# Optimization experiments

Hardware: AMD Instinct MI355X
Metric: run time of the kernel (lower is better)

Reference implementation:

```python
import jax, jax.numpy as jnp
import numpy as np

B, C_IN, IMG = 4, 1, 256
E, P = 800, 4            # embed_size, patch_size
H, DH, M = 8, 64, 64     # heads, dim_head=heads**2, num_landmarks
N = (IMG // P) ** 2      # 4096 tokens
OUT = 256                # output_size
RESK = 33                # lucidrains residual depthwise conv kernel
BN_EPS = 1e-5
LN_EPS = 1e-5
PINV_ITERS = 6


def setup_inputs() -> dict:
    key = jax.random.key(0)
    ks = iter(jax.random.split(key, 32))
    def nrm(shape, s=0.02):
        return jax.random.normal(next(ks), shape, jnp.float32) * s
    inp = {"x": jax.random.normal(next(ks), (B, C_IN, IMG, IMG), jnp.float32)}
    # conv stack: (in, out, kernel); last conv has stride=P, padding=0
    for i, (ci, co, kk) in enumerate([(C_IN, 64, 3), (64, 128, 3), (128, 256, 3), (256, E, P)]):
        inp[f"w{i}"] = nrm((co, ci, kk, kk), 0.05)
        inp[f"b{i}"] = jnp.zeros((co,), jnp.float32)
        inp[f"g{i}"] = jnp.ones((co,), jnp.float32)    # BN gamma
        inp[f"be{i}"] = jnp.zeros((co,), jnp.float32)  # BN beta
        inp[f"mu{i}"] = nrm((co,), 0.1)                # BN running mean
        inp[f"var{i}"] = jax.random.uniform(next(ks), (co,), jnp.float32, 0.5, 1.5)
    inp["qkv_w"] = nrm((E, 3 * H * DH))      # to_qkv (no bias)
    inp["out_w"] = nrm((H * DH, E))          # to_out linear
    inp["out_b"] = jnp.zeros((E,), jnp.float32)
    inp["res_w"] = nrm((H, 1, RESK, 1), 0.05)  # depthwise residual conv over token dim
    inp["ln_g"] = jnp.ones((E,), jnp.float32)
    inp["ln_b"] = jnp.zeros((E,), jnp.float32)
    inp["head_w"] = nrm((E, OUT * OUT // N))   # Linear(800, 16)
    inp["head_b"] = jnp.zeros((OUT * OUT // N,), jnp.float32)
    return inp


def conv2d(x, w, b, stride, pad):
    y = jax.lax.conv_general_dilated(x, w, (stride, stride), [(pad, pad), (pad, pad)],
                                     dimension_numbers=("NCHW", "OIHW", "NCHW"))
    return y + b[None, :, None, None]


def bn(x, g, be, mu, var):
    s = g * jax.lax.rsqrt(var + BN_EPS)  # eval-mode BatchNorm
    return x * s[None, :, None, None] + (be - mu * s)[None, :, None, None]


def moore_penrose_pinv(a, iters=PINV_ITERS):
    I = jnp.eye(a.shape[-1], dtype=a.dtype)
    z = jnp.swapaxes(a, -1, -2) / (jnp.max(jnp.abs(a).sum(-1)) * jnp.max(jnp.abs(a).sum(-2)))
    for _ in range(iters):
        az = a @ z
        z = 0.25 * z @ (13.0 * I - az @ (15.0 * I - az @ (7.0 * I - az)))
    return z


def reference(x, w0, b0, g0, be0, mu0, var0, w1, b1, g1, be1, mu1, var1,
              w2, b2, g2, be2, mu2, var2, w3, b3, g3, be3, mu3, var3,
              qkv_w, out_w, out_b, res_w, ln_g, ln_b, head_w, head_b):
    # ---- PatchEmbedConv ----
    h = x
    blocks = [(w0, b0, g0, be0, mu0, var0, 1, 1), (w1, b1, g1, be1, mu1, var1, 1, 1),
              (w2, b2, g2, be2, mu2, var2, 1, 1), (w3, b3, g3, be3, mu3, var3, P, 0)]
    for w, b, g, be, mu, var, st, pd in blocks:
        h = jax.nn.relu(bn(conv2d(h, w, b, st, pd), g, be, mu, var))
    tok = h.reshape(B, E, N).transpose(0, 2, 1)  # [B, N, E]

    # ---- NystromAttention (n % m == 0, so no front padding needed) ----
    qkv = tok @ qkv_w  # [B, N, 3*H*DH]
    q, k, v = [t.reshape(B, N, H, DH).transpose(0, 2, 1, 3) for t in jnp.split(qkv, 3, axis=-1)]
    q = q * (DH ** -0.5)
    l = N // M
    q_l = q.reshape(B, H, M, l, DH).mean(3)  # landmark means over consecutive blocks
    k_l = k.reshape(B, H, M, l, DH).mean(3)
    a1 = jax.nn.softmax(jnp.einsum("bhnd,bhmd->bhnm", q, k_l), axis=-1)    # [B,H,N,M]
    a2 = jax.nn.softmax(jnp.einsum("bhmd,bhkd->bhmk", q_l, k_l), axis=-1)  # [B,H,M,M]
    a3 = jax.nn.softmax(jnp.einsum("bhmd,bhnd->bhmn", q_l, k), axis=-1)    # [B,H,M,N]
    out = (a1 @ moore_penrose_pinv(a2)) @ (a3 @ v)  # [B,H,N,DH]
    # residual depthwise conv over the token dim of v (groups = heads)
    res = jax.lax.conv_general_dilated(v, res_w, (1, 1), [(RESK // 2, RESK // 2), (0, 0)],
                                       dimension_numbers=("NCHW", "OIHW", "NCHW"),
                                       feature_group_count=H)
    out = out + res
    out = out.transpose(0, 2, 1, 3).reshape(B, N, H * DH)
    out = out @ out_w + out_b  # [B, N, E]

    # ---- LayerNorm ----
    mu_t = out.mean(-1, keepdims=True)
    var_t = out.var(-1, keepdims=True)
    out = (out - mu_t) * jax.lax.rsqrt(var_t + LN_EPS) * ln_g + ln_b

    # ---- reconstruction head ----
    y = jax.nn.sigmoid(out @ head_w + head_b)  # [B, N, OUT*OUT/N]
    return y.reshape(-1, 1, OUT, OUT)
```

## Files before the change

### kernel.cpp

```cpp
#include <hip/hip_runtime.h>

#define DI __device__ __forceinline__

constexpr float BN_EPS_C = 1e-5f;
constexpr float LN_EPS_C = 1e-5f;

typedef _Float16 half8 __attribute__((ext_vector_type(8)));
typedef float f32x4 __attribute__((ext_vector_type(4)));

constexpr size_t B_H0   = 0;
constexpr size_t B_H1   = 8388608;
constexpr size_t B_H2   = 25165824;
constexpr size_t B_Q    = 25165824;
constexpr size_t B_K    = 41943040;
constexpr size_t B_V    = 58720256;
constexpr size_t B_KT   = 75497472;
constexpr size_t B_ATT  = 92274688;
constexpr size_t B_LNB  = 25165824;
constexpr size_t B_TOK  = 159383552;
constexpr size_t B_WP1  = 185597952;
constexpr size_t B_WP2  = 185745408;
constexpr size_t B_WP3  = 186335232;
constexpr size_t B_QKVT = 192888832;
constexpr size_t B_OWT  = 195346432;
constexpr size_t B_QL   = 196165632;
constexpr size_t B_KL   = 196689920;
constexpr size_t B_KLH  = 197214208;
constexpr size_t B_A2   = 197476352;
constexpr size_t B_PV   = 198000640;
constexpr size_t B_W2T  = 198524928;
constexpr size_t B_A3V  = 198787072;
constexpr size_t B_SCAL = 199311360;
constexpr size_t B_HWH  = 199311424;

DI float blockReduceSum(float v) {
  #pragma unroll
  for (int o = 32; o; o >>= 1) v += __shfl_xor(v, o);
  __shared__ float red[4];
  int w = threadIdx.x >> 6;
  __syncthreads();
  if ((threadIdx.x & 63) == 0) red[w] = v;
  __syncthreads();
  return red[0] + red[1] + red[2] + red[3];
}

template <int LP, int RP>
DI void mm16(const float* L, const float* R, int r0, int c0, float reg[4][4]) {
  #pragma unroll
  for (int i = 0; i < 4; ++i)
    #pragma unroll
    for (int j = 0; j < 4; ++j) reg[i][j] = 0.f;
  for (int dd = 0; dd < 64; ++dd) {
    float l[4], r[4];
    #pragma unroll
    for (int i = 0; i < 4; ++i) l[i] = L[(size_t)(r0 + i) * LP + dd];
    #pragma unroll
    for (int j = 0; j < 4; ++j) r[j] = R[(size_t)dd * RP + c0 + j];
    #pragma unroll
    for (int i = 0; i < 4; ++i)
      #pragma unroll
      for (int j = 0; j < 4; ++j) reg[i][j] = fmaf(l[i], r[j], reg[i][j]);
  }
}

__global__ void k_init(float* scal) {
  if (threadIdx.x < 2) scal[threadIdx.x] = 0.f;
}

__global__ void k_pack_w(const float* __restrict__ src, _Float16* __restrict__ dst,
                         int CO, int CI, int Q) {
  int i = blockIdx.x * 256 + threadIdx.x;
  if (i >= CO * CI * Q) return;
  int q = i % Q, ci = (i / Q) % CI, co = i / (Q * CI);
  dst[((size_t)co * Q + q) * CI + ci] = (_Float16)src[i];
}

__global__ void k_pack_t(const float* __restrict__ src, _Float16* __restrict__ dst,
                         int K, int N) {
  int i = blockIdx.x * 256 + threadIdx.x;
  if (i >= K * N) return;
  int n = i % N, k = i / N;
  dst[(size_t)n * K + k] = (_Float16)src[i];
}

__global__ __launch_bounds__(256) void k_conv0(
    const float* __restrict__ xb, const float* __restrict__ w0, const float* __restrict__ b0,
    const float* __restrict__ g0, const float* __restrict__ be0, const float* __restrict__ mu0,
    const float* __restrict__ var0, _Float16* __restrict__ h0) {
  const int t = threadIdx.x, co = t & 63, xg = t >> 6;
  const int y = blockIdx.x;
  float wreg[9];
  #pragma unroll
  for (int q = 0; q < 9; ++q) wreg[q] = w0[co * 9 + q];
  float s = g0[co] * rsqrtf(var0[co] + BN_EPS_C);
  float sh = fmaf(b0[co] - mu0[co], s, be0[co]);
  for (int xl = 0; xl < 64; ++xl) {
    int xx = xg * 64 + xl;
    float acc = 0.f;
    #pragma unroll
    for (int dy = 0; dy < 3; ++dy) {
      int yy = y + dy - 1;
      if ((unsigned)yy >= 256u) continue;
      #pragma unroll
      for (int dx = 0; dx < 3; ++dx) {
        int xi = xx + dx - 1;
        if ((unsigned)xi >= 256u) continue;
        acc = fmaf(wreg[dy * 3 + dx], xb[yy * 256 + xi], acc);
      }
    }
    float v = fmaxf(fmaf(acc, s, sh), 0.f);
    h0[((size_t)y * 256 + xx) * 64 + co] = (_Float16)v;
  }
}

template <int CI>
__global__ __launch_bounds__(256) void k_convs(
    const _Float16* __restrict__ in, const _Float16* __restrict__ wp,
    const float* __restrict__ bias, const float* __restrict__ g, const float* __restrict__ be,
    const float* __restrict__ mu, const float* __restrict__ var,
    _Float16* __restrict__ out, int CO, int NCT) {
  __shared__ _Float16 Ab[2][128 * 40];
  __shared__ _Float16 Bb[2][128 * 40];
  constexpr int CPQ = CI / 32;
  constexpr int NCK = 9 * CPQ;
  const int t = threadIdx.x;
  const int bid = blockIdx.x;
  const int xcd = bid & 7, slot = bid >> 3;
  const int pj = slot / NCT, cc = slot % NCT;
  const int p = pj * 8 + xcd;
  const int r0 = p * 128, c0 = cc * 128;

  const int ma = t >> 2, kga = t & 3;
  int ry[2], rx[2];
  #pragma unroll
  for (int s = 0; s < 2; ++s) {
    int r = r0 + ma + s * 64;
    ry[s] = r >> 8;
    rx[s] = r & 255;
  }
  const _Float16* baseB[2];
  #pragma unroll
  for (int s = 0; s < 2; ++s)
    baseB[s] = wp + (size_t)(c0 + ma + s * 64) * 9 * CI + kga * 8;
  const int wo = ma * 40 + kga * 8;

  auto loadA = [&](int s, int ck) -> half8 {
    int q = ck / CPQ, coff = (ck % CPQ) * 32;
    int yy = ry[s] + q / 3 - 1;
    int xx = rx[s] + q % 3 - 1;
    half8 a = {};
    if ((unsigned)yy < 256u && (unsigned)xx < 256u)
      a = *reinterpret_cast<const half8*>(in + ((size_t)yy * 256 + xx) * CI + coff + kga * 8);
    return a;
  };

  {
    half8 a0 = loadA(0, 0), a1 = loadA(1, 0);
    half8 b0v = *reinterpret_cast<const half8*>(baseB[0]);
    half8 b1v = *reinterpret_cast<const half8*>(baseB[1]);
    *reinterpret_cast<half8*>(&Ab[0][wo]) = a0;
    *reinterpret_cast<half8*>(&Ab[0][wo + 2560]) = a1;
    *reinterpret_cast<half8*>(&Bb[0][wo]) = b0v;
    *reinterpret_cast<half8*>(&Bb[0][wo + 2560]) = b1v;
  }
  __syncthreads();

  const int w = t >> 6, lo = t & 15, hi = (t >> 4) & 3;
  const int wm = w >> 1, wn = w & 1;
  const int roA = (wm * 64 + lo) * 40 + 8 * hi;
  const int roB = (wn * 64 + lo) * 40 + 8 * hi;
  f32x4 acc[4][4] = {};

  for (int ck = 0; ck < NCK; ++ck) {
    const int cur = ck & 1;
    const bool more = (ck + 1 < NCK);
    half8 rA0, rA1, rB0, rB1;
    if (more) {
      rA0 = loadA(0, ck + 1);
      rA1 = loadA(1, ck + 1);
      rB0 = *reinterpret_cast<const half8*>(baseB[0] + (ck + 1) * 32);
      rB1 = *reinterpret_cast<const half8*>(baseB[1] + (ck + 1) * 32);
    }
    half8 af[4], bf[4];
    #pragma unroll
    for (int mi = 0; mi < 4; ++mi)
      af[mi] = *reinterpret_cast<const half8*>(&Ab[cur][roA + mi * 640]);
    #pragma unroll
    for (int ni = 0; ni < 4; ++ni)
      bf[ni] = *reinterpret_cast<const half8*>(&Bb[cur][roB + ni * 640]);
    #pragma unroll
    for (int mi = 0; mi < 4; ++mi)
      #pragma unroll
      for (int ni = 0; ni < 4; ++ni)
        acc[mi][ni] = __builtin_amdgcn_mfma_f32_16x16x32_f16(af[mi], bf[ni], acc[mi][ni], 0, 0, 0);
    if (more) {
      *reinterpret_cast<half8*>(&Ab[cur ^ 1][wo]) = rA0;
      *reinterpret_cast<half8*>(&Ab[cur ^ 1][wo + 2560]) = rA1;
      *reinterpret_cast<half8*>(&Bb[cur ^ 1][wo]) = rB0;
      *reinterpret_cast<half8*>(&Bb[cur ^ 1][wo + 2560]) = rB1;
    }
    __syncthreads();
  }

  #pragma unroll
  for (int ni = 0; ni < 4; ++ni) {
    int co = c0 + wn * 64 + ni * 16 + lo;
    float s = g[co] * rsqrtf(var[co] + BN_EPS_C);
    float sh = fmaf(bias[co] - mu[co], s, be[co]);
    #pragma unroll
    for (int mi = 0; mi < 4; ++mi)
      #pragma unroll
      for (int rr = 0; rr < 4; ++rr) {
        int row = r0 + wm * 64 + mi * 16 + hi * 4 + rr;
        float v = fmaxf(fmaf(acc[mi][ni][rr], s, sh), 0.f);
        out[(size_t)row * CO + co] = (_Float16)v;
      }
  }
}

__global__ __launch_bounds__(256) void k_c3(
    const _Float16* __restrict__ h2, const _Float16* __restrict__ wp3,
    const float* __restrict__ b3, const float* __restrict__ g3, const float* __restrict__ be3,
    const float* __restrict__ mu3, const float* __restrict__ var3,
    _Float16* __restrict__ tok) {
  __shared__ _Float16 Abuf[2][128 * 40];
  __shared__ _Float16 Bbuf[2][160 * 40];
  const int t = threadIdx.x;
  const int bid = blockIdx.x;
  const int xcd = bid & 7, slot = bid >> 3;
  const int pj = slot / 5, cc = slot % 5;
  const int p = pj * 8 + xcd;
  const int r0 = p * 128, c0 = cc * 160;
  const int img = r0 >> 12;
  const _Float16* h2i = h2 + (size_t)img * 16777216;

  const int ma = t >> 2, kga = t & 3;
  const _Float16* baseA[2];
  #pragma unroll
  for (int s = 0; s < 2; ++s) {
    int m = ma + s * 64;
    int r = r0 + m;
    int py = (r & 4095) >> 6, px = r & 63;
    baseA[s] = h2i + ((size_t)py * 1024 + px * 4) * 256 + kga * 8;
  }
  const _Float16* baseB[3];
  #pragma unroll
  for (int s = 0; s < 3; ++s) {
    int cb = ma + s * 64;
    baseB[s] = wp3 + (size_t)(c0 + (cb < 160 ? cb : 159)) * 4096 + kga * 8;
  }
  const int wo = ma * 40 + kga * 8;

  const int w = t >> 6, lo = t & 15, hi = (t >> 4) & 3;
  const int wm = w >> 1, wn = w & 1;
  const int roA = (wm * 64 + lo) * 40 + 8 * hi;
  const int roB = (wn * 80 + lo) * 40 + 8 * hi;

  f32x4 acc[4][5] = {};

  {
    half8 a0 = *reinterpret_cast<const half8*>(baseA[0]);
    half8 a1 = *reinterpret_cast<const half8*>(baseA[1]);
    half8 b0v = *reinterpret_cast<const half8*>(baseB[0]);
    half8 b1v = *reinterpret_cast<const half8*>(baseB[1]);
    *reinterpret_cast<half8*>(&Abuf[0][wo]) = a0;
    *reinterpret_cast<half8*>(&Abuf[0][wo + 2560]) = a1;
    *reinterpret_cast<half8*>(&Bbuf[0][wo]) = b0v;
    *reinterpret_cast<half8*>(&Bbuf[0][wo + 2560]) = b1v;
    if (t < 128) {
      half8 b2v = *reinterpret_cast<const half8*>(baseB[2]);
      *reinterpret_cast<half8*>(&Bbuf[0][wo + 5120]) = b2v;
    }
  }
  __syncthreads();

  for (int ck = 0; ck < 128; ++ck) {
    const int cur = ck & 1;
    const bool more = (ck + 1 < 128);
    half8 rA0, rA1, rB0, rB1, rB2;
    if (more) {
      const int kn = (ck + 1) << 5;
      const int q = kn >> 8, qk = kn & 255;
      const int aoff = (q >> 2) * 65536 + (q & 3) * 256 + qk;
      rA0 = *reinterpret_cast<const half8*>(baseA[0] + aoff);
      rA1 = *reinterpret_cast<const half8*>(baseA[1] + aoff);
      rB0 = *reinterpret_cast<const half8*>(baseB[0] + kn);
      rB1 = *reinterpret_cast<const half8*>(baseB[1] + kn);
      if (t < 128) rB2 = *reinterpret_cast<const half8*>(baseB[2] + kn);
    }
    half8 af[4], bf[5];
    #pragma unroll
    for (int mi = 0; mi < 4; ++mi)
      af[mi] = *reinterpret_cast<const half8*>(&Abuf[cur][roA + mi * 640]);
    #pragma unroll
    for (int ni = 0; ni < 5; ++ni)
      bf[ni] = *reinterpret_cast<const half8*>(&Bbuf[cur][roB + ni * 640]);
    #pragma unroll
    for (int mi = 0; mi < 4; ++mi)
      #pragma unroll
      for (int ni = 0; ni < 5; ++ni)
        acc[mi][ni] = __builtin_amdgcn_mfma_f32_16x16x32_f16(af[mi], bf[ni], acc[mi][ni], 0, 0, 0);
    if (more) {
      *reinterpret_cast<half8*>(&Abuf[cur ^ 1][wo]) = rA0;
      *reinterpret_cast<half8*>(&Abuf[cur ^ 1][wo + 2560]) = rA1;
      *reinterpret_cast<half8*>(&Bbuf[cur ^ 1][wo]) = rB0;
      *reinterpret_cast<half8*>(&Bbuf[cur ^ 1][wo + 2560]) = rB1;
      if (t < 128) *reinterpret_cast<half8*>(&Bbuf[cur ^ 1][wo + 5120]) = rB2;
    }
    __syncthreads();
  }

  #pragma unroll
  for (int ni = 0; ni < 5; ++ni) {
    int col = c0 + wn * 80 + ni * 16 + lo;
    float s = g3[col] * rsqrtf(var3[col] + BN_EPS_C);
    float sh = fmaf(b3[col] - mu3[col], s, be3[col]);
    #pragma unroll
    for (int mi = 0; mi < 4; ++mi)
      #pragma unroll
      for (int rr = 0; rr < 4; ++rr) {
        int row = r0 + wm * 64 + mi * 16 + hi * 4 + rr;
        float v = fmaxf(fmaf(acc[mi][ni][rr], s, sh), 0.f);
        tok[(size_t)row * 800 + col] = (_Float16)v;
      }
  }
}

__global__ __launch_bounds__(256) void k_qkv_s(
    const _Float16* __restrict__ tok, const _Float16* __restrict__ qkvT,
    _Float16* __restrict__ qx, _Float16* __restrict__ kx, _Float16* __restrict__ vx) {
  __shared__ _Float16 Ab[2][128 * 40];
  __shared__ _Float16 Bb[2][128 * 40];
  const int t = threadIdx.x;
  const int bid = blockIdx.x;
  const int xcd = bid & 7, slot = bid >> 3;
  const int pj = slot / 12, cc = slot % 12;
  const int p = pj * 8 + xcd;
  const int r0 = p * 128, c0 = cc * 128;

  const int ma = t >> 2, kga = t & 3;
  const _Float16* baseA[2];
  const _Float16* baseB[2];
  #pragma unroll
  for (int s = 0; s < 2; ++s) {
    baseA[s] = tok + (size_t)(r0 + ma + s * 64) * 800 + kga * 8;
    baseB[s] = qkvT + (size_t)(c0 + ma + s * 64) * 800 + kga * 8;
  }
  const int wo = ma * 40 + kga * 8;

  {
    half8 a0 = *reinterpret_cast<const half8*>(baseA[0]);
    half8 a1 = *reinterpret_cast<const half8*>(baseA[1]);
    half8 b0v = *reinterpret_cast<const half8*>(baseB[0]);
    half8 b1v = *reinterpret_cast<const half8*>(baseB[1]);
    *reinterpret_cast<half8*>(&Ab[0][wo]) = a0;
    *reinterpret_cast<half8*>(&Ab[0][wo + 2560]) = a1;
    *reinterpret_cast<half8*>(&Bb[0][wo]) = b0v;
    *reinterpret_cast<half8*>(&Bb[0][wo + 2560]) = b1v;
  }
  __syncthreads();

  const int w = t >> 6, lo = t & 15, hi = (t >> 4) & 3;
  const int wm = w >> 1, wn = w & 1;
  const int roA = (wm * 64 + lo) * 40 + 8 * hi;
  const int roB = (wn * 64 + lo) * 40 + 8 * hi;
  f32x4 acc[4][4] = {};

  for (int ck = 0; ck < 25; ++ck) {
    const int cur = ck & 1;
    const bool more = (ck + 1 < 25);
    half8 rA0, rA1, rB0, rB1;
    if (more) {
      const int kn = (ck + 1) * 32;
      rA0 = *reinterpret_cast<const half8*>(baseA[0] + kn);
      rA1 = *reinterpret_cast<const half8*>(baseA[1] + kn);
      rB0 = *reinterpret_cast<const half8*>(baseB[0] + kn);
      rB1 = *reinterpret_cast<const half8*>(baseB[1] + kn);
    }
    half8 af[4], bf[4];
    #pragma unroll
    for (int mi = 0; mi < 4; ++mi)
      af[mi] = *reinterpret_cast<const half8*>(&Ab[cur][roA + mi * 640]);
    #pragma unroll
    for (int ni = 0; ni < 4; ++ni)
      bf[ni] = *reinterpret_cast<const half8*>(&Bb[cur][roB + ni * 640]);
    #pragma unroll
    for (int mi = 0; mi < 4; ++mi)
      #pragma unroll
      for (int ni = 0; ni < 4; ++ni)
        acc[mi][ni] = __builtin_amdgcn_mfma_f32_16x16x32_f16(af[mi], bf[ni], acc[mi][ni], 0, 0, 0);
    if (more) {
      *reinterpret_cast<half8*>(&Ab[cur ^ 1][wo]) = rA0;
      *reinterpret_cast<half8*>(&Ab[cur ^ 1][wo + 2560]) = rA1;
      *reinterpret_cast<half8*>(&Bb[cur ^ 1][wo]) = rB0;
      *reinterpret_cast<half8*>(&Bb[cur ^ 1][wo + 2560]) = rB1;
    }
    __syncthreads();
  }

  const int seg = cc >> 2;
  const float scale = (seg == 0) ? 0.125f : 1.0f;
  _Float16* dst = (seg == 0) ? qx : (seg == 1) ? kx : vx;
  #pragma unroll
  for (int ni = 0; ni < 4; ++ni) {
    int cseg = (cc & 3) * 128 + wn * 64 + ni * 16 + lo;
    int h = cseg >> 6, d = cseg & 63;
    #pragma unroll
    for (int mi = 0; mi < 4; ++mi)
      #pragma unroll
      for (int rr = 0; rr < 4; ++rr) {
        int row = r0 + wm * 64 + mi * 16 + hi * 4 + rr;
        int b = row >> 12, nn = row & 4095;
        dst[((size_t)(b * 8 + h) * 4096 + nn) * 64 + d] = (_Float16)(acc[mi][ni][rr] * scale);
      }
  }
}

__global__ __launch_bounds__(256) void k_op_s(
    const _Float16* __restrict__ attb, const _Float16* __restrict__ owT,
    const float* __restrict__ ob, _Float16* __restrict__ lnb) {
  __shared__ _Float16 Abuf[2][128 * 40];
  __shared__ _Float16 Bbuf[2][160 * 40];
  const int t = threadIdx.x;
  const int bid = blockIdx.x;
  const int xcd = bid & 7, slot = bid >> 3;
  const int pj = slot / 5, cc = slot % 5;
  const int p = pj * 8 + xcd;
  const int r0 = p * 128, c0 = cc * 160;

  const int ma = t >> 2, kga = t & 3;
  const _Float16* baseA[2];
  #pragma unroll
  for (int s = 0; s < 2; ++s)
    baseA[s] = attb + (size_t)(r0 + ma + s * 64) * 512 + kga * 8;
  const _Float16* baseB[3];
  #pragma unroll
  for (int s = 0; s < 3; ++s) {
    int cb = ma + s * 64;
    baseB[s] = owT + (size_t)(c0 + (cb < 160 ? cb : 159)) * 512 + kga * 8;
  }
  const int wo = ma * 40 + kga * 8;

  const int w = t >> 6, lo = t & 15, hi = (t >> 4) & 3;
  const int wm = w >> 1, wn = w & 1;
  const int roA = (wm * 64 + lo) * 40 + 8 * hi;
  const int roB = (wn * 80 + lo) * 40 + 8 * hi;

  f32x4 acc[4][5] = {};

  {
    half8 a0 = *reinterpret_cast<const half8*>(baseA[0]);
    half8 a1 = *reinterpret_cast<const half8*>(baseA[1]);
    half8 b0v = *reinterpret_cast<const half8*>(baseB[0]);
    half8 b1v = *reinterpret_cast<const half8*>(baseB[1]);
    *reinterpret_cast<half8*>(&Abuf[0][wo]) = a0;
    *reinterpret_cast<half8*>(&Abuf[0][wo + 2560]) = a1;
    *reinterpret_cast<half8*>(&Bbuf[0][wo]) = b0v;
    *reinterpret_cast<half8*>(&Bbuf[0][wo + 2560]) = b1v;
    if (t < 128) {
      half8 b2v = *reinterpret_cast<const half8*>(baseB[2]);
      *reinterpret_cast<half8*>(&Bbuf[0][wo + 5120]) = b2v;
    }
  }
  __syncthreads();

  for (int ck = 0; ck < 16; ++ck) {
    const int cur = ck & 1;
    const bool more = (ck + 1 < 16);
    half8 rA0, rA1, rB0, rB1, rB2;
    if (more) {
      const int kn = (ck + 1) << 5;
      rA0 = *reinterpret_cast<const half8*>(baseA[0] + kn);
      rA1 = *reinterpret_cast<const half8*>(baseA[1] + kn);
      rB0 = *reinterpret_cast<const half8*>(baseB[0] + kn);
      rB1 = *reinterpret_cast<const half8*>(baseB[1] + kn);
      if (t < 128) rB2 = *reinterpret_cast<const half8*>(baseB[2] + kn);
    }
    half8 af[4], bf[5];
    #pragma unroll
    for (int mi = 0; mi < 4; ++mi)
      af[mi] = *reinterpret_cast<const half8*>(&Abuf[cur][roA + mi * 640]);
    #pragma unroll
    for (int ni = 0; ni < 5; ++ni)
      bf[ni] = *reinterpret_cast<const half8*>(&Bbuf[cur][roB + ni * 640]);
    #pragma unroll
    for (int mi = 0; mi < 4; ++mi)
      #pragma unroll
      for (int ni = 0; ni < 5; ++ni)
        acc[mi][ni] = __builtin_amdgcn_mfma_f32_16x16x32_f16(af[mi], bf[ni], acc[mi][ni], 0, 0, 0);
    if (more) {
      *reinterpret_cast<half8*>(&Abuf[cur ^ 1][wo]) = rA0;
      *reinterpret_cast<half8*>(&Abuf[cur ^ 1][wo + 2560]) = rA1;
      *reinterpret_cast<half8*>(&Bbuf[cur ^ 1][wo]) = rB0;
      *reinterpret_cast<half8*>(&Bbuf[cur ^ 1][wo + 2560]) = rB1;
      if (t < 128) *reinterpret_cast<half8*>(&Bbuf[cur ^ 1][wo + 5120]) = rB2;
    }
    __syncthreads();
  }

  #pragma unroll
  for (int ni = 0; ni < 5; ++ni) {
    int col = c0 + wn * 80 + ni * 16 + lo;
    float bv = ob[col];
    #pragma unroll
    for (int mi = 0; mi < 4; ++mi)
      #pragma unroll
      for (int rr = 0; rr < 4; ++rr) {
        int row = r0 + wm * 64 + mi * 16 + hi * 4 + rr;
        lnb[(size_t)row * 800 + col] = (_Float16)(acc[mi][ni][rr] + bv);
      }
  }
}

__global__ __launch_bounds__(256) void k_transpose(const _Float16* __restrict__ kx,
                                                   _Float16* __restrict__ kT) {
  __shared__ _Float16 tile[64 * 66];
  const int bh = blockIdx.y, n0 = blockIdx.x * 64;
  const _Float16* src = kx + ((size_t)bh * 4096 + n0) * 64;
  const int t = threadIdx.x;
  #pragma unroll
  for (int u = 0; u < 16; ++u) {
    int e = t + u * 256;
    int r = e >> 6, d = e & 63;
    tile[d * 66 + r] = src[e];
  }
  __syncthreads();
  _Float16* dst = kT + (size_t)bh * 262144 + n0;
  #pragma unroll
  for (int u = 0; u < 16; ++u) {
    int e = t + u * 256;
    int d = e >> 6, j = e & 63;
    dst[(size_t)d * 4096 + j] = tile[d * 66 + j];
  }
}

__global__ __launch_bounds__(64) void k_landmark(
    const _Float16* __restrict__ qx, const _Float16* __restrict__ kx,
    float* __restrict__ ql, float* __restrict__ kl, _Float16* __restrict__ klh) {
  const int d = threadIdx.x;
  const int m = blockIdx.x, bh = blockIdx.y;
  const _Float16* qp = qx + ((size_t)bh * 4096 + m * 64) * 64 + d;
  const _Float16* kp = kx + ((size_t)bh * 4096 + m * 64) * 64 + d;
  float sq = 0.f, sk = 0.f;
  #pragma unroll 8
  for (int j = 0; j < 64; ++j) {
    sq += (float)qp[(size_t)j * 64];
    sk += (float)kp[(size_t)j * 64];
  }
  sq *= (1.f / 64.f);
  sk *= (1.f / 64.f);
  ql[((size_t)bh * 64 + m) * 64 + d] = sq;
  kl[((size_t)bh * 64 + m) * 64 + d] = sk;
  klh[((size_t)bh * 64 + m) * 64 + d] = (_Float16)sk;
}

__global__ __launch_bounds__(64) void k_a2(
    const float* __restrict__ ql, const float* __restrict__ kl,
    float* __restrict__ a2, float* __restrict__ scal) {
  __shared__ float sp[64 * 65];
  const int bh = blockIdx.x, t = threadIdx.x;
  const float* qr = ql + ((size_t)bh * 64 + t) * 64;
  const float* kb = kl + (size_t)bh * 4096;
  float mx = -1e30f;
  for (int c = 0; c < 64; ++c) {
    float acc = 0.f;
    #pragma unroll 8
    for (int dd = 0; dd < 64; ++dd) acc = fmaf(qr[dd], kb[c * 64 + dd], acc);
    sp[t * 65 + c] = acc;
    mx = fmaxf(mx, acc);
  }
  float sum = 0.f;
  for (int c = 0; c < 64; ++c) {
    float e = expf(sp[t * 65 + c] - mx);
    sp[t * 65 + c] = e;
    sum += e;
  }
  float inv = 1.f / sum;
  float rs = 0.f;
  for (int c = 0; c < 64; ++c) {
    float p = sp[t * 65 + c] * inv;
    sp[t * 65 + c] = p;
    a2[(size_t)bh * 4096 + t * 64 + c] = p;
    rs += p;
  }
  atomicMax(reinterpret_cast<int*>(scal), __float_as_int(rs));
  __syncthreads();
  float cs = 0.f;
  for (int r = 0; r < 64; ++r) cs += sp[r * 65 + t];
  atomicMax(reinterpret_cast<int*>(scal) + 1, __float_as_int(cs));
}

__global__ __launch_bounds__(256) void k_a3v(
    const float* __restrict__ ql, const _Float16* __restrict__ kT,
    const _Float16* __restrict__ vx, float* __restrict__ a3v) {
  __shared__ float sq[64];
  __shared__ float sP[4096];
  __shared__ float red[4];
  __shared__ float red2[4][64];
  const int t = threadIdx.x;
  const int m = blockIdx.x, bh = blockIdx.y;
  if (t < 64) sq[t] = ql[((size_t)bh * 64 + m) * 64 + t];
  __syncthreads();
  const _Float16* kb = kT + (size_t)bh * 262144;
  float sc[16];
  #pragma unroll
  for (int i = 0; i < 16; ++i) sc[i] = 0.f;
  for (int dd = 0; dd < 64; ++dd) {
    float qv = sq[dd];
    const _Float16* kr = kb + (size_t)dd * 4096 + t;
    #pragma unroll
    for (int i = 0; i < 16; ++i) sc[i] = fmaf(qv, (float)kr[i * 256], sc[i]);
  }
  float mx = sc[0];
  #pragma unroll
  for (int i = 1; i < 16; ++i) mx = fmaxf(mx, sc[i]);
  #pragma unroll
  for (int o = 32; o; o >>= 1) mx = fmaxf(mx, __shfl_xor(mx, o));
  if ((t & 63) == 0) red[t >> 6] = mx;
  __syncthreads();
  mx = fmaxf(fmaxf(red[0], red[1]), fmaxf(red[2], red[3]));
  __syncthreads();
  float sum = 0.f;
  #pragma unroll
  for (int i = 0; i < 16; ++i) {
    sc[i] = expf(sc[i] - mx);
    sum += sc[i];
  }
  #pragma unroll
  for (int o = 32; o; o >>= 1) sum += __shfl_xor(sum, o);
  if ((t & 63) == 0) red[t >> 6] = sum;
  __syncthreads();
  sum = red[0] + red[1] + red[2] + red[3];
  float inv = 1.f / sum;
  #pragma unroll
  for (int i = 0; i < 16; ++i) sP[t + i * 256] = sc[i] * inv;
  __syncthreads();
  const int d = t & 63, seg = t >> 6;
  const _Float16* vb = vx + (size_t)bh * 262144;
  float acc = 0.f;
  for (int n = seg * 1024; n < seg * 1024 + 1024; ++n)
    acc = fmaf(sP[n], (float)vb[(size_t)n * 64 + d], acc);
  red2[seg][d] = acc;
  __syncthreads();
  if (seg == 0)
    a3v[((size_t)bh * 64 + m) * 64 + d] = red2[0][d] + red2[1][d] + red2[2][d] + red2[3][d];
}

__global__ __launch_bounds__(256) void k_pinv(
    const float* __restrict__ a2g, const float* __restrict__ scal, float* __restrict__ pv) {
  __shared__ float z[64 * 65];
  __shared__ float az[64 * 65];
  __shared__ float tb[64 * 65];
  const int bh = blockIdx.x, t = threadIdx.x;
  const int r0 = (t >> 4) << 2, c0 = (t & 15) << 2;
  const float* ag = a2g + (size_t)bh * 4096;
  const float denom = 1.f / (scal[0] * scal[1]);
  #pragma unroll
  for (int i = 0; i < 4; ++i)
    #pragma unroll
    for (int j = 0; j < 4; ++j)
      z[(r0 + i) * 65 + c0 + j] = ag[(c0 + j) * 64 + r0 + i] * denom;
  __syncthreads();
  float reg[4][4], val[4][4];
  for (int it = 0; it < 6; ++it) {
    mm16<64, 65>(ag, z, r0, c0, reg);
    #pragma unroll
    for (int i = 0; i < 4; ++i)
      #pragma unroll
      for (int j = 0; j < 4; ++j) az[(r0 + i) * 65 + c0 + j] = reg[i][j];
    __syncthreads();
    mm16<65, 65>(az, az, r0, c0, reg);
    #pragma unroll
    for (int i = 0; i < 4; ++i)
      #pragma unroll
      for (int j = 0; j < 4; ++j)
        tb[(r0 + i) * 65 + c0 + j] = 7.f * az[(r0 + i) * 65 + c0 + j] - reg[i][j];
    __syncthreads();
    mm16<65, 65>(az, tb, r0, c0, reg);
    #pragma unroll
    for (int i = 0; i < 4; ++i)
      #pragma unroll
      for (int j = 0; j < 4; ++j)
        val[i][j] = 15.f * az[(r0 + i) * 65 + c0 + j] - reg[i][j];
    __syncthreads();
    #pragma unroll
    for (int i = 0; i < 4; ++i)
      #pragma unroll
      for (int j = 0; j < 4; ++j) tb[(r0 + i) * 65 + c0 + j] = val[i][j];
    __syncthreads();
    mm16<65, 65>(z, tb, r0, c0, reg);
    #pragma unroll
    for (int i = 0; i < 4; ++i)
      #pragma unroll
      for (int j = 0; j < 4; ++j)
        val[i][j] = 0.25f * (13.f * z[(r0 + i) * 65 + c0 + j] - reg[i][j]);
    __syncthreads();
    #pragma unroll
    for (int i = 0; i < 4; ++i)
      #pragma unroll
      for (int j = 0; j < 4; ++j) z[(r0 + i) * 65 + c0 + j] = val[i][j];
    __syncthreads();
  }
  #pragma unroll
  for (int i = 0; i < 4; ++i)
    #pragma unroll
    for (int j = 0; j < 4; ++j)
      pv[(size_t)bh * 4096 + (r0 + i) * 64 + c0 + j] = z[(r0 + i) * 65 + c0 + j];
}

__global__ __launch_bounds__(256) void k_w2(
    const float* __restrict__ pv, const float* __restrict__ a3v, _Float16* __restrict__ w2t) {
  const int bh = blockIdx.x, t = threadIdx.x;
  const int r0 = (t >> 4) << 2, c0 = (t & 15) << 2;
  float reg[4][4];
  mm16<64, 64>(pv + (size_t)bh * 4096, a3v + (size_t)bh * 4096, r0, c0, reg);
  #pragma unroll
  for (int i = 0; i < 4; ++i)
    #pragma unroll
    for (int j = 0; j < 4; ++j)
      w2t[(size_t)bh * 4096 + (c0 + j) * 64 + (r0 + i)] = (_Float16)reg[i][j];
}

__global__ __launch_bounds__(256) void k_combine_m(
    const _Float16* __restrict__ qx, const _Float16* __restrict__ klh,
    const _Float16* __restrict__ w2t, const _Float16* __restrict__ vx,
    const float* __restrict__ rw, _Float16* __restrict__ att) {
  __shared__ _Float16 sP[64 * 72];
  __shared__ _Float16 sVT[64 * 104];
  __shared__ _Float16 sT[64 * 104];
  __shared__ float sR[33];
  const int t = threadIdx.x, w = t >> 6, lo = t & 15, hi = (t >> 4) & 3;
  const int n0 = blockIdx.x * 64;
  const int h = blockIdx.y, b = blockIdx.z, bh = b * 8 + h;
  if (t < 33) sR[t] = rw[h * 33 + t];
  __syncthreads();
  const _Float16* vb = vx + (size_t)bh * 262144;
  #pragma unroll
  for (int u = 0; u < 24; ++u) {
    int e = t + u * 256;
    int r = e >> 6, d = e & 63;
    int nn = n0 - 16 + r;
    sVT[d * 104 + r] = ((unsigned)nn < 4096u) ? vb[(size_t)nn * 64 + d] : (_Float16)0.f;
  }
  #pragma unroll
  for (int u = 0; u < 24; ++u) {
    int e = t + u * 256;
    int r = e % 96, i = e / 96;
    int j = r - i;
    sT[i * 104 + r] = (j >= 0 && j < 33) ? (_Float16)sR[j] : (_Float16)0.f;
  }
  f32x4 sa[4] = {};
  const _Float16* qp = qx + ((size_t)bh * 4096 + n0 + w * 16 + lo) * 64 + 8 * hi;
  const _Float16* klp = klh + (size_t)bh * 4096;
  #pragma unroll
  for (int c = 0; c < 2; ++c) {
    half8 a = *reinterpret_cast<const half8*>(qp + 32 * c);
    #pragma unroll
    for (int ct = 0; ct < 4; ++ct) {
      half8 bf = *reinterpret_cast<const half8*>(klp + (size_t)(ct * 16 + lo) * 64 + 8 * hi + 32 * c);
      sa[ct] = __builtin_amdgcn_mfma_f32_16x16x32_f16(a, bf, sa[ct], 0, 0, 0);
    }
  }
  #pragma unroll
  for (int r = 0; r < 4; ++r) {
    float mx = fmaxf(fmaxf(sa[0][r], sa[1][r]), fmaxf(sa[2][r], sa[3][r]));
    #pragma unroll
    for (int o = 8; o; o >>= 1) mx = fmaxf(mx, __shfl_xor(mx, o));
    float e0 = expf(sa[0][r] - mx), e1 = expf(sa[1][r] - mx);
    float e2 = expf(sa[2][r] - mx), e3 = expf(sa[3][r] - mx);
    float sm = e0 + e1 + e2 + e3;
    #pragma unroll
    for (int o = 8; o; o >>= 1) sm += __shfl_xor(sm, o);
    float inv = 1.f / sm;
    int row = w * 16 + hi * 4 + r;
    sP[row * 72 + lo] = (_Float16)(e0 * inv);
    sP[row * 72 + 16 + lo] = (_Float16)(e1 * inv);
    sP[row * 72 + 32 + lo] = (_Float16)(e2 * inv);
    sP[row * 72 + 48 + lo] = (_Float16)(e3 * inv);
  }
  __syncthreads();
  f32x4 ao[4] = {};
  const _Float16* w2p = w2t + (size_t)bh * 4096;
  #pragma unroll
  for (int c = 0; c < 2; ++c) {
    half8 a = *reinterpret_cast<const half8*>(&sP[(w * 16 + lo) * 72 + 8 * hi + 32 * c]);
    #pragma unroll
    for (int ct = 0; ct < 4; ++ct) {
      half8 bf = *reinterpret_cast<const half8*>(w2p + (size_t)(ct * 16 + lo) * 64 + 8 * hi + 32 * c);
      ao[ct] = __builtin_amdgcn_mfma_f32_16x16x32_f16(a, bf, ao[ct], 0, 0, 0);
    }
  }
  #pragma unroll
  for (int c = 0; c < 3; ++c) {
    half8 a = *reinterpret_cast<const half8*>(&sT[(w * 16 + lo) * 104 + 8 * hi + 32 * c]);
    #pragma unroll
    for (int ct = 0; ct < 4; ++ct) {
      half8 bf = *reinterpret_cast<const half8*>(&sVT[(ct * 16 + lo) * 104 + 8 * hi + 32 * c]);
      ao[ct] = __builtin_amdgcn_mfma_f32_16x16x32_f16(a, bf, ao[ct], 0, 0, 0);
    }
  }
  _Float16* ab = att + ((size_t)b * 4096) * 512 + (size_t)h * 64;
  #pragma unroll
  for (int ct = 0; ct < 4; ++ct)
    #pragma unroll
    for (int r = 0; r < 4; ++r) {
      int n = n0 + w * 16 + hi * 4 + r;
      ab[(size_t)n * 512 + ct * 16 + lo] = (_Float16)ao[ct][r];
    }
}

__global__ __launch_bounds__(256) void k_ln16(
    _Float16* __restrict__ buf, const float* __restrict__ g, const float* __restrict__ bb) {
  const int t = threadIdx.x;
  _Float16* p = buf + (size_t)blockIdx.x * 800;
  float x0 = (float)p[t], x1 = (float)p[t + 256], x2 = (float)p[t + 512];
  float x3 = (t < 32) ? (float)p[t + 768] : 0.f;
  float s = blockReduceSum(x0 + x1 + x2 + x3);
  float mean = s * (1.f / 800.f);
  float d0 = x0 - mean, d1 = x1 - mean, d2 = x2 - mean;
  float d3 = (t < 32) ? x3 - mean : 0.f;
  float s2 = blockReduceSum(d0 * d0 + d1 * d1 + d2 * d2 + d3 * d3);
  float rstd = rsqrtf(s2 * (1.f / 800.f) + LN_EPS_C);
  p[t] = (_Float16)(d0 * rstd * g[t] + bb[t]);
  p[t + 256] = (_Float16)(d1 * rstd * g[t + 256] + bb[t + 256]);
  p[t + 512] = (_Float16)(d2 * rstd * g[t + 512] + bb[t + 512]);
  if (t < 32) p[t + 768] = (_Float16)(d3 * rstd * g[t + 768] + bb[t + 768]);
}

__global__ __launch_bounds__(256) void k_head_m(
    const _Float16* __restrict__ ln, const _Float16* __restrict__ hwh,
    const float* __restrict__ hb, float* __restrict__ out) {
  const int t = threadIdx.x, w = t >> 6, lo = t & 15, hi = (t >> 4) & 3;
  const int row0 = blockIdx.x * 64 + w * 16;
  const _Float16* ap = ln + (size_t)(row0 + lo) * 800 + 8 * hi;
  const _Float16* bp = hwh + (size_t)lo * 800 + 8 * hi;
  f32x4 acc = {};
  #pragma unroll 5
  for (int k = 0; k < 800; k += 32) {
    half8 a = *reinterpret_cast<const half8*>(ap + k);
    half8 b = *reinterpret_cast<const half8*>(bp + k);
    acc = __builtin_amdgcn_mfma_f32_16x16x32_f16(a, b, acc, 0, 0, 0);
  }
  float bv = hb[lo];
  #pragma unroll
  for (int r = 0; r < 4; ++r) {
    int row = row0 + hi * 4 + r;
    out[(size_t)row * 16 + lo] = 1.f / (1.f + expf(-(acc[r] + bv)));
  }
}

extern "C" void kernel_launch(void* const* d_in, const int* in_sizes, int n_in,
                              void* d_out, int out_size, void* d_ws, size_t ws_size,
                              hipStream_t stream) {
  (void)in_sizes; (void)n_in; (void)out_size; (void)ws_size;
  const float* x     = (const float*)d_in[0];
  const float* w0    = (const float*)d_in[1];
  const float* b0    = (const float*)d_in[2];
  const float* g0    = (const float*)d_in[3];
  const float* be0   = (const float*)d_in[4];
  const float* mu0   = (const float*)d_in[5];
  const float* var0  = (const float*)d_in[6];
  const float* w1    = (const float*)d_in[7];
  const float* b1    = (const float*)d_in[8];
  const float* g1    = (const float*)d_in[9];
  const float* be1   = (const float*)d_in[10];
  const float* mu1   = (const float*)d_in[11];
  const float* var1  = (const float*)d_in[12];
  const float* w2c   = (const float*)d_in[13];
  const float* b2    = (const float*)d_in[14];
  const float* g2    = (const float*)d_in[15];
  const float* be2   = (const float*)d_in[16];
  const float* mu2   = (const float*)d_in[17];
  const float* var2  = (const float*)d_in[18];
  const float* w3    = (const float*)d_in[19];
  const float* b3    = (const float*)d_in[20];
  const float* g3    = (const float*)d_in[21];
  const float* be3   = (const float*)d_in[22];
  const float* mu3   = (const float*)d_in[23];
  const float* var3  = (const float*)d_in[24];
  const float* qkvw  = (const float*)d_in[25];
  const float* outw  = (const float*)d_in[26];
  const float* outbv = (const float*)d_in[27];
  const float* resw  = (const float*)d_in[28];
  const float* lng   = (const float*)d_in[29];
  const float* lnbv  = (const float*)d_in[30];
  const float* headw = (const float*)d_in[31];
  const float* headb = (const float*)d_in[32];

  char* wsb = (char*)d_ws;
  _Float16* h0   = (_Float16*)(wsb + B_H0);
  _Float16* h1   = (_Float16*)(wsb + B_H1);
  _Float16* h2   = (_Float16*)(wsb + B_H2);
  _Float16* qb   = (_Float16*)(wsb + B_Q);
  _Float16* kb   = (_Float16*)(wsb + B_K);
  _Float16* vb   = (_Float16*)(wsb + B_V);
  _Float16* kT   = (_Float16*)(wsb + B_KT);
  _Float16* tok  = (_Float16*)(wsb + B_TOK);
  _Float16* attb = (_Float16*)(wsb + B_ATT);
  _Float16* wp1  = (_Float16*)(wsb + B_WP1);
  _Float16* wp2  = (_Float16*)(wsb + B_WP2);
  _Float16* wp3  = (_Float16*)(wsb + B_WP3);
  _Float16* qkvT = (_Float16*)(wsb + B_QKVT);
  _Float16* owT  = (_Float16*)(wsb + B_OWT);
  _Float16* klh  = (_Float16*)(wsb + B_KLH);
  _Float16* w2t  = (_Float16*)(wsb + B_W2T);
  _Float16* hwh  = (_Float16*)(wsb + B_HWH);
  _Float16* lnb16 = (_Float16*)(wsb + B_LNB);
  float* ql   = (float*)(wsb + B_QL);
  float* kl   = (float*)(wsb + B_KL);
  float* a2   = (float*)(wsb + B_A2);
  float* pv   = (float*)(wsb + B_PV);
  float* a3v  = (float*)(wsb + B_A3V);
  float* scal = (float*)(wsb + B_SCAL);

  k_pack_w<<<(128 * 64 * 9 + 255) / 256, 256, 0, stream>>>(w1, wp1, 128, 64, 9);
  k_pack_w<<<(256 * 128 * 9 + 255) / 256, 256, 0, stream>>>(w2c, wp2, 256, 128, 9);
  k_pack_w<<<(800 * 256 * 16 + 255) / 256, 256, 0, stream>>>(w3, wp3, 800, 256, 16);
  k_pack_t<<<(800 * 1536 + 255) / 256, 256, 0, stream>>>(qkvw, qkvT, 800, 1536);
  k_pack_t<<<(512 * 800 + 255) / 256, 256, 0, stream>>>(outw, owT, 512, 800);
  k_pack_t<<<(800 * 16 + 255) / 256, 256, 0, stream>>>(headw, hwh, 800, 16);
  k_init<<<1, 64, 0, stream>>>(scal);

  for (int img = 0; img < 4; ++img) {
    k_conv0<<<dim3(256), 256, 0, stream>>>(
        x + (size_t)img * 65536, w0, b0, g0, be0, mu0, var0, h0);
    k_convs<64><<<dim3(512), 256, 0, stream>>>(
        h0, wp1, b1, g1, be1, mu1, var1, h1, 128, 1);
    k_convs<128><<<dim3(1024), 256, 0, stream>>>(
        h1, wp2, b2, g2, be2, mu2, var2, h2 + (size_t)img * 16777216, 256, 2);
  }
  k_c3<<<dim3(640), 256, 0, stream>>>(h2, wp3, b3, g3, be3, mu3, var3, tok);
  k_qkv_s<<<dim3(1536), 256, 0, stream>>>(tok, qkvT, qb, kb, vb);
  k_transpose<<<dim3(64, 32), 256, 0, stream>>>(kb, kT);
  k_landmark<<<dim3(64, 32), 64, 0, stream>>>(qb, kb, ql, kl, klh);
  k_a2<<<dim3(32), 64, 0, stream>>>(ql, kl, a2, scal);
  k_a3v<<<dim3(64, 32), 256, 0, stream>>>(ql, kT, vb, a3v);
  k_pinv<<<dim3(32), 256, 0, stream>>>(a2, scal, pv);
  k_w2<<<dim3(32), 256, 0, stream>>>(pv, a3v, w2t);
  k_combine_m<<<dim3(64, 8, 4), 256, 0, stream>>>(qb, klh, w2t, vb, resw, attb);
  k_op_s<<<dim3(640), 256, 0, stream>>>(attb, owT, outbv, lnb16);
  k_ln16<<<dim3(16384), 256, 0, stream>>>(lnb16, lng, lnbv);
  k_head_m<<<dim3(256), 256, 0, stream>>>(lnb16, hwh, headb, (float*)d_out);
}
```

Baseline: 1.162 ms.

## Fuse weight packing, write K transposed from QKV GEMM, merge pinv with W2

Merges the six weight-packing kernels and the scalar init into one launch. The QKV GEMM now writes K straight into the transposed [bh,d,n] layout, which removes the separate transpose kernel and the K buffer, and the landmark kernel reads K from that layout with vector loads. The pinv kernel also does the pinv×a3v product from shared memory, which removes the k_w2 launch and the pv round trip. The risk is the QKV epilogue for K, where scattered stores with a 4096 stride may coalesce poorly.

```diff
diff --git a/kernel.cpp b/kernel.cpp
--- a/kernel.cpp
+++ b/kernel.cpp
@@ -12,7 +12,6 @@
 constexpr size_t B_H1   = 8388608;
 constexpr size_t B_H2   = 25165824;
 constexpr size_t B_Q    = 25165824;
-constexpr size_t B_K    = 41943040;
 constexpr size_t B_V    = 58720256;
 constexpr size_t B_KT   = 75497472;
 constexpr size_t B_ATT  = 92274688;
@@ -27,7 +26,6 @@
 constexpr size_t B_KL   = 196689920;
 constexpr size_t B_KLH  = 197214208;
 constexpr size_t B_A2   = 197476352;
-constexpr size_t B_PV   = 198000640;
 constexpr size_t B_W2T  = 198524928;
 constexpr size_t B_A3V  = 198787072;
 constexpr size_t B_SCAL = 199311360;
@@ -63,24 +61,39 @@
   }
 }
 
-__global__ void k_init(float* scal) {
-  if (threadIdx.x < 2) scal[threadIdx.x] = 0.f;
-}
-
-__global__ void k_pack_w(const float* __restrict__ src, _Float16* __restrict__ dst,
-                         int CO, int CI, int Q) {
-  int i = blockIdx.x * 256 + threadIdx.x;
-  if (i >= CO * CI * Q) return;
-  int q = i % Q, ci = (i / Q) % CI, co = i / (Q * CI);
-  dst[((size_t)co * Q + q) * CI + ci] = (_Float16)src[i];
-}
-
-__global__ void k_pack_t(const float* __restrict__ src, _Float16* __restrict__ dst,
-                         int K, int N) {
-  int i = blockIdx.x * 256 + threadIdx.x;
-  if (i >= K * N) return;
-  int n = i % N, k = i / N;
-  dst[(size_t)n * K + k] = (_Float16)src[i];
+__global__ void k_pack_all(
+    const float* __restrict__ w1, const float* __restrict__ w2c, const float* __restrict__ w3,
+    const float* __restrict__ qkvw, const float* __restrict__ outw, const float* __restrict__ headw,
+    _Float16* __restrict__ wp1, _Float16* __restrict__ wp2, _Float16* __restrict__ wp3,
+    _Float16* __restrict__ qkvT, _Float16* __restrict__ owT, _Float16* __restrict__ hwh,
+    float* __restrict__ scal) {
+  size_t i = (size_t)blockIdx.x * 256 + threadIdx.x;
+  if (i < 73728) {
+    int q = i % 9, ci = (i / 9) % 64, co = i / (9 * 64);
+    wp1[((size_t)co * 9 + q) * 64 + ci] = (_Float16)w1[i];
+  } else if (i < 368640) {
+    size_t j = i - 73728;
+    int q = j % 9, ci = (j / 9) % 128, co = j / (9 * 128);
+    wp2[((size_t)co * 9 + q) * 128 + ci] = (_Float16)w2c[j];
+  } else if (i < 3645440) {
+    size_t j = i - 368640;
+    int q = j % 16, ci = (j / 16) % 256, co = j / (16 * 256);
+    wp3[((size_t)co * 16 + q) * 256 + ci] = (_Float16)w3[j];
+  } else if (i < 4874240) {
+    size_t j = i - 3645440;
+    int n = j % 1536, k = j / 1536;
+    qkvT[(size_t)n * 800 + k] = (_Float16)qkvw[j];
+  } else if (i < 5283840) {
+    size_t j = i - 4874240;
+    int n = j % 800, k = j / 800;
+    owT[(size_t)n * 512 + k] = (_Float16)outw[j];
+  } else if (i < 5296640) {
+    size_t j = i - 5283840;
+    int n = j % 16, k = j / 16;
+    hwh[(size_t)n * 800 + k] = (_Float16)headw[j];
+  } else if (i < 5296642) {
+    scal[i - 5296640] = 0.f;
+  }
 }
 
 __global__ __launch_bounds__(256) void k_conv0(
@@ -328,7 +341,7 @@
 
 __global__ __launch_bounds__(256) void k_qkv_s(
     const _Float16* __restrict__ tok, const _Float16* __restrict__ qkvT,
-    _Float16* __restrict__ qx, _Float16* __restrict__ kx, _Float16* __restrict__ vx) {
+    _Float16* __restrict__ qx, _Float16* __restrict__ kTg, _Float16* __restrict__ vx) {
   __shared__ _Float16 Ab[2][128 * 40];
   __shared__ _Float16 Bb[2][128 * 40];
   const int t = threadIdx.x;
@@ -399,20 +412,36 @@
   }
 
   const int seg = cc >> 2;
-  const float scale = (seg == 0) ? 0.125f : 1.0f;
-  _Float16* dst = (seg == 0) ? qx : (seg == 1) ? kx : vx;
-  #pragma unroll
-  for (int ni = 0; ni < 4; ++ni) {
-    int cseg = (cc & 3) * 128 + wn * 64 + ni * 16 + lo;
-    int h = cseg >> 6, d = cseg & 63;
-    #pragma unroll
-    for (int mi = 0; mi < 4; ++mi)
-      #pragma unroll
-      for (int rr = 0; rr < 4; ++rr) {
-        int row = r0 + wm * 64 + mi * 16 + hi * 4 + rr;
-        int b = row >> 12, nn = row & 4095;
-        dst[((size_t)(b * 8 + h) * 4096 + nn) * 64 + d] = (_Float16)(acc[mi][ni][rr] * scale);
-      }
+  if (seg == 1) {
+    #pragma unroll
+    for (int ni = 0; ni < 4; ++ni) {
+      int cseg = (cc & 3) * 128 + wn * 64 + ni * 16 + lo;
+      int h = cseg >> 6, d = cseg & 63;
+      #pragma unroll
+      for (int mi = 0; mi < 4; ++mi)
+        #pragma unroll
+        for (int rr = 0; rr < 4; ++rr) {
+          int row = r0 + wm * 64 + mi * 16 + hi * 4 + rr;
+          int b = row >> 12, nn = row & 4095;
+          kTg[((size_t)(b * 8 + h) * 64 + d) * 4096 + nn] = (_Float16)acc[mi][ni][rr];
+        }
+    }
+  } else {
+    const float scale = (seg == 0) ? 0.125f : 1.0f;
+    _Float16* dst = (seg == 0) ? qx : vx;
+    #pragma unroll
+    for (int ni = 0; ni < 4; ++ni) {
+      int cseg = (cc & 3) * 128 + wn * 64 + ni * 16 + lo;
+      int h = cseg >> 6, d = cseg & 63;
+      #pragma unroll
+      for (int mi = 0; mi < 4; ++mi)
+        #pragma unroll
+        for (int rr = 0; rr < 4; ++rr) {
+          int row = r0 + wm * 64 + mi * 16 + hi * 4 + rr;
+          int b = row >> 12, nn = row & 4095;
+          dst[((size_t)(b * 8 + h) * 4096 + nn) * 64 + d] = (_Float16)(acc[mi][ni][rr] * scale);
+        }
+    }
   }
 }
 
@@ -512,40 +541,21 @@
   }
 }
 
-__global__ __launch_bounds__(256) void k_transpose(const _Float16* __restrict__ kx,
-                                                   _Float16* __restrict__ kT) {
-  __shared__ _Float16 tile[64 * 66];
-  const int bh = blockIdx.y, n0 = blockIdx.x * 64;
-  const _Float16* src = kx + ((size_t)bh * 4096 + n0) * 64;
-  const int t = threadIdx.x;
-  #pragma unroll
-  for (int u = 0; u < 16; ++u) {
-    int e = t + u * 256;
-    int r = e >> 6, d = e & 63;
-    tile[d * 66 + r] = src[e];
-  }
-  __syncthreads();
-  _Float16* dst = kT + (size_t)bh * 262144 + n0;
-  #pragma unroll
-  for (int u = 0; u < 16; ++u) {
-    int e = t + u * 256;
-    int d = e >> 6, j = e & 63;
-    dst[(size_t)d * 4096 + j] = tile[d * 66 + j];
-  }
-}
-
 __global__ __launch_bounds__(64) void k_landmark(
-    const _Float16* __restrict__ qx, const _Float16* __restrict__ kx,
+    const _Float16* __restrict__ qx, const _Float16* __restrict__ kT,
     float* __restrict__ ql, float* __restrict__ kl, _Float16* __restrict__ klh) {
   const int d = threadIdx.x;
   const int m = blockIdx.x, bh = blockIdx.y;
   const _Float16* qp = qx + ((size_t)bh * 4096 + m * 64) * 64 + d;
-  const _Float16* kp = kx + ((size_t)bh * 4096 + m * 64) * 64 + d;
+  const _Float16* kp = kT + ((size_t)bh * 64 + d) * 4096 + m * 64;
   float sq = 0.f, sk = 0.f;
   #pragma unroll 8
-  for (int j = 0; j < 64; ++j) {
-    sq += (float)qp[(size_t)j * 64];
-    sk += (float)kp[(size_t)j * 64];
+  for (int j = 0; j < 64; ++j) sq += (float)qp[(size_t)j * 64];
+  #pragma unroll
+  for (int j = 0; j < 64; j += 8) {
+    half8 kv = *reinterpret_cast<const half8*>(kp + j);
+    #pragma unroll
+    for (int u = 0; u < 8; ++u) sk += (float)kv[u];
   }
   sq *= (1.f / 64.f);
   sk *= (1.f / 64.f);
@@ -647,7 +657,8 @@
 }
 
 __global__ __launch_bounds__(256) void k_pinv(
-    const float* __restrict__ a2g, const float* __restrict__ scal, float* __restrict__ pv) {
+    const float* __restrict__ a2g, const float* __restrict__ scal,
+    const float* __restrict__ a3vg, _Float16* __restrict__ w2t) {
   __shared__ float z[64 * 65];
   __shared__ float az[64 * 65];
   __shared__ float tb[64 * 65];
@@ -701,19 +712,7 @@
       for (int j = 0; j < 4; ++j) z[(r0 + i) * 65 + c0 + j] = val[i][j];
     __syncthreads();
   }
-  #pragma unroll
-  for (int i = 0; i < 4; ++i)
-    #pragma unroll
-    for (int j = 0; j < 4; ++j)
-      pv[(size_t)bh * 4096 + (r0 + i) * 64 + c0 + j] = z[(r0 + i) * 65 + c0 + j];
-}
-
-__global__ __launch_bounds__(256) void k_w2(
-    const float* __restrict__ pv, const float* __restrict__ a3v, _Float16* __restrict__ w2t) {
-  const int bh = blockIdx.x, t = threadIdx.x;
-  const int r0 = (t >> 4) << 2, c0 = (t & 15) << 2;
-  float reg[4][4];
-  mm16<64, 64>(pv + (size_t)bh * 4096, a3v + (size_t)bh * 4096, r0, c0, reg);
+  mm16<65, 64>(z, a3vg + (size_t)bh * 4096, r0, c0, reg);
   #pragma unroll
   for (int i = 0; i < 4; ++i)
     #pragma unroll
@@ -892,7 +891,6 @@
   _Float16* h1   = (_Float16*)(wsb + B_H1);
   _Float16* h2   = (_Float16*)(wsb + B_H2);
   _Float16* qb   = (_Float16*)(wsb + B_Q);
-  _Float16* kb   = (_Float16*)(wsb + B_K);
   _Float16* vb   = (_Float16*)(wsb + B_V);
   _Float16* kT   = (_Float16*)(wsb + B_KT);
   _Float16* tok  = (_Float16*)(wsb + B_TOK);
@@ -909,17 +907,11 @@
   float* ql   = (float*)(wsb + B_QL);
   float* kl   = (float*)(wsb + B_KL);
   float* a2   = (float*)(wsb + B_A2);
-  float* pv   = (float*)(wsb + B_PV);
   float* a3v  = (float*)(wsb + B_A3V);
   float* scal = (float*)(wsb + B_SCAL);
 
-  k_pack_w<<<(128 * 64 * 9 + 255) / 256, 256, 0, stream>>>(w1, wp1, 128, 64, 9);
-  k_pack_w<<<(256 * 128 * 9 + 255) / 256, 256, 0, stream>>>(w2c, wp2, 256, 128, 9);
-  k_pack_w<<<(800 * 256 * 16 + 255) / 256, 256, 0, stream>>>(w3, wp3, 800, 256, 16);
-  k_pack_t<<<(800 * 1536 + 255) / 256, 256, 0, stream>>>(qkvw, qkvT, 800, 1536);
-  k_pack_t<<<(512 * 800 + 255) / 256, 256, 0, stream>>>(outw, owT, 512, 800);
-  k_pack_t<<<(800 * 16 + 255) / 256, 256, 0, stream>>>(headw, hwh, 800, 16);
-  k_init<<<1, 64, 0, stream>>>(scal);
+  k_pack_all<<<dim3(20691), 256, 0, stream>>>(
+      w1, w2c, w3, qkvw, outw, headw, wp1, wp2, wp3, qkvT, owT, hwh, scal);
 
   for (int img = 0; img < 4; ++img) {
     k_conv0<<<dim3(256), 256, 0, stream>>>(
@@ -930,13 +922,11 @@
         h1, wp2, b2, g2, be2, mu2, var2, h2 + (size_t)img * 16777216, 256, 2);
   }
   k_c3<<<dim3(640), 256, 0, stream>>>(h2, wp3, b3, g3, be3, mu3, var3, tok);
-  k_qkv_s<<<dim3(1536), 256, 0, stream>>>(tok, qkvT, qb, kb, vb);
-  k_transpose<<<dim3(64, 32), 256, 0, stream>>>(kb, kT);
-  k_landmark<<<dim3(64, 32), 64, 0, stream>>>(qb, kb, ql, kl, klh);
+  k_qkv_s<<<dim3(1536), 256, 0, stream>>>(tok, qkvT, qb, kT, vb);
+  k_landmark<<<dim3(64, 32), 64, 0, stream>>>(qb, kT, ql, kl, klh);
   k_a2<<<dim3(32), 64, 0, stream>>>(ql, kl, a2, scal);
   k_a3v<<<dim3(64, 32), 256, 0, stream>>>(ql, kT, vb, a3v);
-  k_pinv<<<dim3(32), 256, 0, stream>>>(a2, scal, pv);
-  k_w2<<<dim3(32), 256, 0, stream>>>(pv, a3v, w2t);
+  k_pinv<<<dim3(32), 256, 0, stream>>>(a2, scal, a3v, w2t);
   k_combine_m<<<dim3(64, 8, 4), 256, 0, stream>>>(qb, klh, w2t, vb, resw, attb);
   k_op_s<<<dim3(640), 256, 0, stream>>>(attb, owT, outbv, lnb16);
   k_ln16<<<dim3(16384), 256, 0, stream>>>(lnb16, lng, lnbv);
```

Measured after the change: 1.153 ms. About the same (-0.8%).
